# Performance work log

Hardware: AMD Instinct MI355X
Metric: run time of the kernel (lower is better)

The kernel has to match this reference:

```python
import jax, jax.numpy as jnp
import numpy as np
import math

DIM = 1024
NUM_HEADS = 16


def setup_inputs() -> dict:
    key = jax.random.key(0)
    ks = jax.random.split(key, 6)
    B, S, D = 2, 2048, DIM
    return {
        "q": jax.random.normal(ks[0], (B, S, D), dtype=jnp.float32),
        "k": jax.random.normal(ks[1], (B, S, D), dtype=jnp.float32),
        "v": jax.random.normal(ks[2], (B, S, D), dtype=jnp.float32),
        "wq": jax.random.normal(ks[3], (D, D), dtype=jnp.float32),
        "wk": jax.random.normal(ks[4], (D, D), dtype=jnp.float32),
        "wv": jax.random.normal(ks[5], (D, D), dtype=jnp.float32),
    }


def reference(q, k, v, wq, wk, wv):
    B, S, D = q.shape
    H = NUM_HEADS
    hd = D // H
    # projections: [B,S,D] @ [D,D]
    qp = (q @ wq).reshape(B, H, S, hd)  # NOTE: direct reshape, as in the original
    kp = (k @ wk).reshape(B, H, S, hd)
    vp = (v @ wv).reshape(B, H, S, hd)
    scale = 1.0 / math.sqrt(D)  # original scales by sqrt(dim), not sqrt(head_dim)
    att = jnp.einsum("bhqd,bhkd->bhqk", qp, kp) * scale  # [B,H,S,S]
    att = jax.nn.softmax(att, axis=-1)
    out = jnp.einsum("bhqk,bhkd->bhqd", att, vp)  # [B,H,S,hd]
    out = out.transpose(0, 2, 1, 3).reshape(B, S, D)
    return out
```

## Files before the change

kernel.cpp:

```cpp
#include <hip/hip_runtime.h>
#include <hip/hip_bf16.h>
#include <stdint.h>

#define DIMD 1024
#define SEQ  2048
#define NH   16
#define MROWS 4096
#define NQ   65536

typedef __bf16 bf16_t;
typedef bf16_t bf16x8 __attribute__((ext_vector_type(8)));
typedef float  f32x4  __attribute__((ext_vector_type(4)));
typedef unsigned short u16;
typedef unsigned short u16x4 __attribute__((ext_vector_type(4)));
typedef unsigned short u16x8 __attribute__((ext_vector_type(8)));
typedef unsigned int   u32;
typedef u32 u32x2 __attribute__((ext_vector_type(2)));

static __device__ __forceinline__ f32x4 mfma16(bf16x8 a, bf16x8 b, f32x4 c) {
    return __builtin_amdgcn_mfma_f32_16x16x32_bf16(a, b, c, 0, 0, 0);
}

static __device__ __forceinline__ float fast_exp2(float x) {
#if __has_builtin(__builtin_amdgcn_exp2f)
    return __builtin_amdgcn_exp2f(x);
#else
    return exp2f(x);
#endif
}

#define GLD16(gsrc, ldst) __builtin_amdgcn_global_load_lds(                    \
    (const __attribute__((address_space(1))) unsigned int*)(gsrc),             \
    (__attribute__((address_space(3))) unsigned int*)(ldst), 16, 0, 0)

static __device__ __forceinline__ void split_bf16(float x, u16& h, u16& l) {
    u32 u = __float_as_uint(x);
    u16 hu = (u16)(u >> 16);
    float xh = __uint_as_float((u32)hu << 16);
    float lo = x - xh;
    h = hu;
    l = (u16)(__float_as_uint(lo) >> 16);
}

static __device__ __forceinline__ u32 pack_bf16(float a, float b) {
    return (__float_as_uint(a) >> 16) | (__float_as_uint(b) & 0xffff0000u);
}
static __device__ __forceinline__ u32 pack_bf16_rn(float a, float b) {
    u32 ua = __float_as_uint(a) + 0x8000u;
    u32 ub = __float_as_uint(b) + 0x8000u;
    return (ua >> 16) | (ub & 0xffff0000u);
}
static __device__ __forceinline__ float bf_to_f(u16 v) {
    return __uint_as_float((u32)v << 16);
}

__global__ __launch_bounds__(256) void transWs3(
    const float* __restrict__ w0, const float* __restrict__ w1, const float* __restrict__ w2,
    u16* __restrict__ WTsH, u16* __restrict__ WTsL) {
    const int z = blockIdx.z;
    const float* W = z == 0 ? w0 : z == 1 ? w1 : w2;
    __shared__ u16 Hs[4096], Ls[4096];
    const int tid = threadIdx.x;
    const int kt = blockIdx.x, nt = blockIdx.y;
    const int n0 = nt * 128, k0 = kt * 32;
    #pragma unroll
    for (int i = 0; i < 4; i++) {
        int f = i * 256 + tid;
        int kr = f >> 5, nc4 = (f & 31) * 4;
        f32x4 w = *(const f32x4*)&W[(size_t)(k0 + kr) * DIMD + n0 + nc4];
        int cc = kr >> 3, e = kr & 7;
        #pragma unroll
        for (int j = 0; j < 4; j++) {
            u16 hh, ll; split_bf16(w[j], hh, ll);
            Hs[cc * 1024 + (nc4 + j) * 8 + e] = hh;
            Ls[cc * 1024 + (nc4 + j) * 8 + e] = ll;
        }
    }
    __syncthreads();
    const size_t base = (size_t)z * (DIMD * DIMD) + (size_t)(nt * 32 + kt) * 4096;
    #pragma unroll
    for (int i = 0; i < 2; i++) {
        int idx = (i * 256 + tid) * 8;
        *(u16x8*)(WTsH + base + idx) = *(const u16x8*)&Hs[idx];
        *(u16x8*)(WTsL + base + idx) = *(const u16x8*)&Ls[idx];
    }
}

__global__ __launch_bounds__(256, 3) void proj6(
    const float* __restrict__ xq, const float* __restrict__ xk, const float* __restrict__ xv,
    const u16* __restrict__ WTsH, const u16* __restrict__ WTsL,
    u16* __restrict__ qh, u16* __restrict__ ql,
    u16* __restrict__ kh, u16* __restrict__ kl,
    u16* __restrict__ vh) {

    const int z = blockIdx.z;
    const float* X = z == 0 ? xq : z == 1 ? xk : xv;
    const u16* BH = WTsH + (size_t)z * (DIMD * DIMD);
    const u16* BL = WTsL + (size_t)z * (DIMD * DIMD);
    u16* outH = z == 0 ? qh : z == 1 ? kh : vh;
    u16* outL = z == 0 ? ql : kl;
    const float oscale = z == 0 ? 0.0450842200278f : 1.0f;

    __shared__ u16 lds[16384];
    u16* AsH = lds;
    u16* AsL = lds + 4096;
    u16* BsH = lds + 8192;
    u16* BsL = lds + 12288;

    const int tid  = threadIdx.x;
    const int lane = tid & 63, wave = tid >> 6;
    const int quad = lane >> 4, l16 = lane & 15;
    const int wy = wave >> 1, wx = wave & 1;
    const int m0 = blockIdx.x * 128;
    const int n0 = blockIdx.y * 128;
    const size_t Bregion0 = (size_t)(blockIdx.y * 32) * 4096;

    f32x4 acc[4][4];
    #pragma unroll
    for (int mt = 0; mt < 4; mt++)
        #pragma unroll
        for (int nt = 0; nt < 4; nt++) acc[mt][nt] = (f32x4)0.0f;

    for (int kt = 0; kt < 32; kt++) {
        const int k0 = kt * 32;
        {
            const size_t rb = Bregion0 + (size_t)kt * 4096;
            int c0 = tid, c1 = 256 + tid;
            GLD16(BH + rb + c0 * 8, &BsH[c0 * 8]);
            GLD16(BH + rb + c1 * 8, &BsH[c1 * 8]);
            GLD16(BL + rb + c0 * 8, &BsL[c0 * 8]);
            GLD16(BL + rb + c1 * 8, &BsL[c1 * 8]);
        }
        #pragma unroll
        for (int i = 0; i < 4; i++) {
            int f = i * 256 + tid;
            int r = f >> 3, c4 = (f & 7) * 4;
            f32x4 a = *(const f32x4*)&X[(size_t)(m0 + r) * DIMD + k0 + c4];
            int cc = c4 >> 3, e = c4 & 7;
            u16x4 h4, l4;
            #pragma unroll
            for (int j = 0; j < 4; j++) {
                u16 hh, ll; split_bf16(a[j], hh, ll);
                h4[j] = hh; l4[j] = ll;
            }
            *(u16x4*)&AsH[(cc * 128 + r) * 8 + e] = h4;
            *(u16x4*)&AsL[(cc * 128 + r) * 8 + e] = l4;
        }
        __syncthreads();

        bf16x8 aH[4], aL[4], bH[4], bL[4];
        #pragma unroll
        for (int mt = 0; mt < 4; mt++) {
            int r = wy * 64 + mt * 16 + l16;
            aH[mt] = *(const bf16x8*)&AsH[(quad * 128 + r) * 8];
            aL[mt] = *(const bf16x8*)&AsL[(quad * 128 + r) * 8];
        }
        #pragma unroll
        for (int nt = 0; nt < 4; nt++) {
            int r = wx * 64 + nt * 16 + l16;
            bH[nt] = *(const bf16x8*)&BsH[(quad * 128 + r) * 8];
            bL[nt] = *(const bf16x8*)&BsL[(quad * 128 + r) * 8];
        }
        #pragma unroll
        for (int mt = 0; mt < 4; mt++)
            #pragma unroll
            for (int nt = 0; nt < 4; nt++) {
                acc[mt][nt] = mfma16(aH[mt], bH[nt], acc[mt][nt]);
                acc[mt][nt] = mfma16(aH[mt], bL[nt], acc[mt][nt]);
                acc[mt][nt] = mfma16(aL[mt], bH[nt], acc[mt][nt]);
            }
        __syncthreads();
    }

    #pragma unroll
    for (int mt = 0; mt < 4; mt++)
        #pragma unroll
        for (int nt = 0; nt < 4; nt++)
            #pragma unroll
            for (int r = 0; r < 4; r++) {
                int row = m0 + wy * 64 + mt * 16 + quad * 4 + r;
                int col = n0 + wx * 64 + nt * 16 + l16;
                u16 hh, ll; split_bf16(acc[mt][nt][r] * oscale, hh, ll);
                outH[(size_t)row * DIMD + col] = hh;
                if (z != 2) outL[(size_t)row * DIMD + col] = ll;
            }
}

__global__ __launch_bounds__(256) void transposeV(
    const u16* __restrict__ vh, u16* __restrict__ vt) {
    __shared__ u16 Ls[64][72];
    const int tid = threadIdx.x;
    const int bh = blockIdx.y;
    const int s0 = blockIdx.x * 64;
    const size_t slab = (size_t)bh * (SEQ * 64);
    #pragma unroll
    for (int i = 0; i < 2; i++) {
        int f = i * 256 + tid;
        int r = f >> 3, c = (f & 7) * 8;
        *(u16x8*)&Ls[r][c] = *(const u16x8*)(vh + slab + (size_t)(s0 + r) * 64 + c);
    }
    __syncthreads();
    #pragma unroll
    for (int i = 0; i < 2; i++) {
        int f = i * 256 + tid;
        int d = f >> 3, j = (f & 7) * 8;
        u16x8 o;
        #pragma unroll
        for (int jj = 0; jj < 8; jj++) o[jj] = Ls[j + jj][d];
        *(u16x8*)(vt + slab + (size_t)d * SEQ + s0 + j) = o;
    }
}

__global__ __launch_bounds__(256, 3) void flash6(
    const u16* __restrict__ qh, const u16* __restrict__ ql,
    const u16* __restrict__ kh, const u16* __restrict__ kl,
    const u16* __restrict__ vt,
    u16* __restrict__ Opart, float* __restrict__ Mpart, float* __restrict__ Lpart) {

    __shared__ u16 KH[64][72], KL[64][72], VTs[64][72];
    __shared__ u16 Ps[4][32][72];

    const int tid  = threadIdx.x;
    const int lane = tid & 63, wv = tid >> 6;
    const int quad = lane >> 4, l16 = lane & 15;
    const int bh = blockIdx.x, z = blockIdx.z;
    const size_t slab = (size_t)bh * (SEQ * 64);
    const int q0 = blockIdx.y * 128 + wv * 32;
    const int jbase = z * 1024;

    bf16x8 qfH[2][2], qfL[2][2];
    #pragma unroll
    for (int mq = 0; mq < 2; mq++) {
        const size_t rb = slab + (size_t)(q0 + mq * 16 + l16) * 64;
        #pragma unroll
        for (int kk = 0; kk < 2; kk++) {
            qfH[mq][kk] = *(const bf16x8*)(qh + rb + kk * 32 + quad * 8);
            qfL[mq][kk] = *(const bf16x8*)(ql + rb + kk * 32 + quad * 8);
        }
    }

    f32x4 O[2][4];
    float M[2] = {-3.0e38f, -3.0e38f}, L[2] = {0.0f, 0.0f};
    #pragma unroll
    for (int mq = 0; mq < 2; mq++)
        #pragma unroll
        for (int nv = 0; nv < 4; nv++) O[mq][nv] = (f32x4)0.0f;

    const int f0 = tid, f1 = 256 + tid;
    const int r0 = f0 >> 3, c0 = (f0 & 7) * 8;
    const int r1 = f1 >> 3, c1 = (f1 & 7) * 8;
    u16x8 s0, s1, s2, s3, s4, s5;

    {
        const int j0 = jbase;
        s0 = *(const u16x8*)(kh + slab + (size_t)(j0 + r0) * 64 + c0);
        s1 = *(const u16x8*)(kh + slab + (size_t)(j0 + r1) * 64 + c1);
        s2 = *(const u16x8*)(kl + slab + (size_t)(j0 + r0) * 64 + c0);
        s3 = *(const u16x8*)(kl + slab + (size_t)(j0 + r1) * 64 + c1);
        s4 = *(const u16x8*)(vt + slab + (size_t)r0 * SEQ + j0 + c0);
        s5 = *(const u16x8*)(vt + slab + (size_t)r1 * SEQ + j0 + c1);
    }
    *(u16x8*)&KH[r0][c0] = s0;  *(u16x8*)&KH[r1][c1] = s1;
    *(u16x8*)&KL[r0][c0] = s2;  *(u16x8*)&KL[r1][c1] = s3;
    *(u16x8*)&VTs[r0][c0] = s4; *(u16x8*)&VTs[r1][c1] = s5;
    __syncthreads();

    for (int t = 0; t < 16; t++) {
        if (t < 15) {
            const int j0 = jbase + (t + 1) * 64;
            s0 = *(const u16x8*)(kh + slab + (size_t)(j0 + r0) * 64 + c0);
            s1 = *(const u16x8*)(kh + slab + (size_t)(j0 + r1) * 64 + c1);
            s2 = *(const u16x8*)(kl + slab + (size_t)(j0 + r0) * 64 + c0);
            s3 = *(const u16x8*)(kl + slab + (size_t)(j0 + r1) * 64 + c1);
            s4 = *(const u16x8*)(vt + slab + (size_t)r0 * SEQ + j0 + c0);
            s5 = *(const u16x8*)(vt + slab + (size_t)r1 * SEQ + j0 + c1);
        }

        f32x4 St[2][4];
        #pragma unroll
        for (int mq = 0; mq < 2; mq++)
            #pragma unroll
            for (int nt = 0; nt < 4; nt++) St[mq][nt] = (f32x4)0.0f;
        #pragma unroll
        for (int nt = 0; nt < 4; nt++) {
            const int rB = nt * 16 + l16;
            #pragma unroll
            for (int kk = 0; kk < 2; kk++) {
                bf16x8 kHf = *(const bf16x8*)&KH[rB][kk * 32 + quad * 8];
                bf16x8 kLf = *(const bf16x8*)&KL[rB][kk * 32 + quad * 8];
                #pragma unroll
                for (int mq = 0; mq < 2; mq++) {
                    St[mq][nt] = mfma16(kHf, qfH[mq][kk], St[mq][nt]);
                    St[mq][nt] = mfma16(kLf, qfH[mq][kk], St[mq][nt]);
                    St[mq][nt] = mfma16(kHf, qfL[mq][kk], St[mq][nt]);
                }
            }
        }

        #pragma unroll
        for (int mq = 0; mq < 2; mq++) {
            float mx = St[mq][0][0];
            #pragma unroll
            for (int nt = 0; nt < 4; nt++)
                #pragma unroll
                for (int r = 0; r < 4; r++) mx = fmaxf(mx, St[mq][nt][r]);
            mx = fmaxf(mx, __shfl_xor(mx, 16));
            mx = fmaxf(mx, __shfl_xor(mx, 32));
            float Mn = M[mq];
            if (__any(mx > Mn)) {
                Mn = fmaxf(Mn, mx);
                float al = fast_exp2(M[mq] - Mn);
                M[mq] = Mn;
                L[mq] *= al;
                #pragma unroll
                for (int nv = 0; nv < 4; nv++) O[mq][nv] *= al;
            }
            float rs = 0.0f;
            #pragma unroll
            for (int nt = 0; nt < 4; nt++)
                #pragma unroll
                for (int r = 0; r < 4; r++) {
                    float p = fast_exp2(St[mq][nt][r] - Mn);
                    St[mq][nt][r] = p;
                    rs += p;
                }
            rs += __shfl_xor(rs, 16);
            rs += __shfl_xor(rs, 32);
            L[mq] += rs;
            #pragma unroll
            for (int nt = 0; nt < 4; nt++) {
                u32x2 d;
                d[0] = pack_bf16(St[mq][nt][0], St[mq][nt][1]);
                d[1] = pack_bf16(St[mq][nt][2], St[mq][nt][3]);
                *(u32x2*)&Ps[wv][mq * 16 + l16][nt * 16 + quad * 4] = d;
            }
        }

        #pragma unroll
        for (int kk = 0; kk < 2; kk++) {
            bf16x8 pB[2];
            #pragma unroll
            for (int mq = 0; mq < 2; mq++)
                pB[mq] = *(const bf16x8*)&Ps[wv][mq * 16 + l16][kk * 32 + quad * 8];
            #pragma unroll
            for (int nv = 0; nv < 4; nv++) {
                bf16x8 vF = *(const bf16x8*)&VTs[nv * 16 + l16][kk * 32 + quad * 8];
                #pragma unroll
                for (int mq = 0; mq < 2; mq++)
                    O[mq][nv] = mfma16(vF, pB[mq], O[mq][nv]);
            }
        }

        __syncthreads();
        if (t < 15) {
            *(u16x8*)&KH[r0][c0] = s0;  *(u16x8*)&KH[r1][c1] = s1;
            *(u16x8*)&KL[r0][c0] = s2;  *(u16x8*)&KL[r1][c1] = s3;
            *(u16x8*)&VTs[r0][c0] = s4; *(u16x8*)&VTs[r1][c1] = s5;
        }
        __syncthreads();
    }

    const int qgb = bh * SEQ + q0;
    #pragma unroll
    for (int mq = 0; mq < 2; mq++) {
        const int qg = qgb + mq * 16 + l16;
        #pragma unroll
        for (int nv = 0; nv < 4; nv++) {
            u32x2 d;
            d[0] = pack_bf16_rn(O[mq][nv][0], O[mq][nv][1]);
            d[1] = pack_bf16_rn(O[mq][nv][2], O[mq][nv][3]);
            *(u32x2*)(Opart + ((size_t)(z * NQ + qg)) * 64 + nv * 16 + quad * 4) = d;
        }
        if (quad == 0) {
            Mpart[z * NQ + qg] = M[mq];
            Lpart[z * NQ + qg] = L[mq];
        }
    }
}

__global__ __launch_bounds__(256) void combineK(
    const u16* __restrict__ Opart, const float* __restrict__ Mpart,
    const float* __restrict__ Lpart, float* __restrict__ out) {
    int idx = blockIdx.x * 256 + threadIdx.x;
    int qg = idx >> 4, c4 = (idx & 15) * 4;
    float M0 = Mpart[qg], M1 = Mpart[NQ + qg];
    float L0 = Lpart[qg], L1 = Lpart[NQ + qg];
    float Ms = fmaxf(M0, M1);
    float w0 = fast_exp2(M0 - Ms), w1 = fast_exp2(M1 - Ms);
    float inv = 1.0f / (w0 * L0 + w1 * L1);
    u16x4 a = *(const u16x4*)&Opart[(size_t)qg * 64 + c4];
    u16x4 b = *(const u16x4*)&Opart[((size_t)NQ + qg) * 64 + c4];
    f32x4 o;
    #pragma unroll
    for (int j = 0; j < 4; j++)
        o[j] = (w0 * bf_to_f(a[j]) + w1 * bf_to_f(b[j])) * inv;
    int bh = qg >> 11, s = qg & 2047;
    int bb = bh >> 4, h = bh & 15;
    *(f32x4*)&out[((size_t)(bb * SEQ + s)) * DIMD + h * 64 + c4] = o;
}

extern "C" void kernel_launch(void* const* d_in, const int* in_sizes, int n_in,
                              void* d_out, int out_size, void* d_ws, size_t ws_size,
                              hipStream_t stream) {
    const float* q  = (const float*)d_in[0];
    const float* k  = (const float*)d_in[1];
    const float* v  = (const float*)d_in[2];
    const float* wq = (const float*)d_in[3];
    const float* wk = (const float*)d_in[4];
    const float* wv = (const float*)d_in[5];
    float* out = (float*)d_out;

    char* ws = (char*)d_ws;
    const size_t MB = 1 << 20;
    u16* qh   = (u16*)(ws + 0 * MB);
    u16* ql   = (u16*)(ws + 8 * MB);
    u16* kh   = (u16*)(ws + 16 * MB);
    u16* kl   = (u16*)(ws + 24 * MB);
    u16* vh   = (u16*)(ws + 32 * MB);
    u16* vt   = (u16*)(ws + 40 * MB);
    u16* WTsH = (u16*)(ws + 48 * MB);
    u16* WTsL = (u16*)(ws + 54 * MB);
    u16*   Opart = (u16*)(ws + 48 * MB);
    float* Mpart = (float*)(ws + 64 * MB);
    float* Lpart = (float*)(ws + 64 * MB + 512 * 1024);

    transWs3<<<dim3(32, 8, 3), 256, 0, stream>>>(wq, wk, wv, WTsH, WTsL);

    proj6<<<dim3(32, 8, 3), 256, 0, stream>>>(
        q, k, v, WTsH, WTsL, qh, ql, kh, kl, vh);

    transposeV<<<dim3(SEQ / 64, 2 * NH), 256, 0, stream>>>(vh, vt);

    flash6<<<dim3(2 * NH, SEQ / 128, 2), 256, 0, stream>>>(
        qh, ql, kh, kl, vt, Opart, Mpart, Lpart);

    combineK<<<dim3(NQ * 16 / 256), 256, 0, stream>>>(Opart, Mpart, Lpart, out);
}
```

Baseline: 270.5 us.

## Double-buffer projection GEMM loads, swizzle A tile LDS, prioritise flash MFMA waves

The projection kernel now prefetches the next K-slice of X into registers and stages the next weight tile into a second LDS buffer while the current tile's MFMAs run. The A tile gets an XOR-swizzled LDS layout to reduce bank conflicts. The flash attention kernel raises wave priority around its MFMA blocks. This adds LDS use (48KB per block), which may lower occupancy under the 3-block launch bound, plus extra register pressure from the prefetched A values.

```diff
diff --git a/kernel.cpp b/kernel.cpp
--- a/kernel.cpp
+++ b/kernel.cpp
@@ -86,7 +86,7 @@
     }
 }
 
-__global__ __launch_bounds__(256, 3) void proj6(
+__global__ __launch_bounds__(256, 3) void proj7(
     const float* __restrict__ xq, const float* __restrict__ xk, const float* __restrict__ xv,
     const u16* __restrict__ WTsH, const u16* __restrict__ WTsL,
     u16* __restrict__ qh, u16* __restrict__ ql,
@@ -101,11 +101,9 @@
     u16* outL = z == 0 ? ql : kl;
     const float oscale = z == 0 ? 0.0450842200278f : 1.0f;
 
-    __shared__ u16 lds[16384];
+    __shared__ u16 lds[24576];
     u16* AsH = lds;
     u16* AsL = lds + 4096;
-    u16* BsH = lds + 8192;
-    u16* BsL = lds + 12288;
 
     const int tid  = threadIdx.x;
     const int lane = tid & 63, wave = tid >> 6;
@@ -115,45 +113,80 @@
     const int n0 = blockIdx.y * 128;
     const size_t Bregion0 = (size_t)(blockIdx.y * 32) * 4096;
 
+    const int rA  = tid >> 2, ccA = tid & 3;
+    const int idxA0 = ccA * 1024 + ((rA ^ (ccA << 1)) * 8);
+    const int idxA1 = idxA0 + 512;
+    const float* Xb0 = X + (size_t)(m0 + rA) * DIMD + ccA * 8;
+    const float* Xb1 = X + (size_t)(m0 + rA + 64) * DIMD + ccA * 8;
+
     f32x4 acc[4][4];
     #pragma unroll
     for (int mt = 0; mt < 4; mt++)
         #pragma unroll
         for (int nt = 0; nt < 4; nt++) acc[mt][nt] = (f32x4)0.0f;
 
+    f32x4 pa0, pa1, pa2, pa3;
+
+#define LOADA(kt) do {                                                         \
+        pa0 = *(const f32x4*)(Xb0 + (kt) * 32);                                \
+        pa1 = *(const f32x4*)(Xb0 + (kt) * 32 + 4);                            \
+        pa2 = *(const f32x4*)(Xb1 + (kt) * 32);                                \
+        pa3 = *(const f32x4*)(Xb1 + (kt) * 32 + 4);                            \
+    } while (0)
+
+#define WRITEA() do {                                                          \
+        u16x8 h, l;                                                            \
+        _Pragma("unroll")                                                      \
+        for (int j = 0; j < 4; j++) {                                          \
+            u16 hh, ll;                                                        \
+            split_bf16(pa0[j], hh, ll); h[j] = hh;     l[j] = ll;              \
+            split_bf16(pa1[j], hh, ll); h[4 + j] = hh; l[4 + j] = ll;          \
+        }                                                                      \
+        *(u16x8*)&AsH[idxA0] = h;                                              \
+        *(u16x8*)&AsL[idxA0] = l;                                              \
+        _Pragma("unroll")                                                      \
+        for (int j = 0; j < 4; j++) {                                          \
+            u16 hh, ll;                                                        \
+            split_bf16(pa2[j], hh, ll); h[j] = hh;     l[j] = ll;              \
+            split_bf16(pa3[j], hh, ll); h[4 + j] = hh; l[4 + j] = ll;          \
+        }                                                                      \
+        *(u16x8*)&AsH[idxA1] = h;                                              \
+        *(u16x8*)&AsL[idxA1] = l;                                              \
+    } while (0)
+
+#define STAGEB(kt, buf) do {                                                   \
+        const size_t rb = Bregion0 + (size_t)(kt) * 4096;                      \
+        u16* BsHd = lds + 8192 + (buf) * 8192;                                 \
+        u16* BsLd = BsHd + 4096;                                               \
+        int c0 = tid, c1 = 256 + tid;                                          \
+        GLD16(BH + rb + c0 * 8, &BsHd[c0 * 8]);                                \
+        GLD16(BH + rb + c1 * 8, &BsHd[c1 * 8]);                                \
+        GLD16(BL + rb + c0 * 8, &BsLd[c0 * 8]);                                \
+        GLD16(BL + rb + c1 * 8, &BsLd[c1 * 8]);                                \
+    } while (0)
+
+    LOADA(0);
+    STAGEB(0, 0);
+    WRITEA();
+    __syncthreads();
+
     for (int kt = 0; kt < 32; kt++) {
-        const int k0 = kt * 32;
-        {
-            const size_t rb = Bregion0 + (size_t)kt * 4096;
-            int c0 = tid, c1 = 256 + tid;
-            GLD16(BH + rb + c0 * 8, &BsH[c0 * 8]);
-            GLD16(BH + rb + c1 * 8, &BsH[c1 * 8]);
-            GLD16(BL + rb + c0 * 8, &BsL[c0 * 8]);
-            GLD16(BL + rb + c1 * 8, &BsL[c1 * 8]);
-        }
-        #pragma unroll
-        for (int i = 0; i < 4; i++) {
-            int f = i * 256 + tid;
-            int r = f >> 3, c4 = (f & 7) * 4;
-            f32x4 a = *(const f32x4*)&X[(size_t)(m0 + r) * DIMD + k0 + c4];
-            int cc = c4 >> 3, e = c4 & 7;
-            u16x4 h4, l4;
-            #pragma unroll
-            for (int j = 0; j < 4; j++) {
-                u16 hh, ll; split_bf16(a[j], hh, ll);
-                h4[j] = hh; l4[j] = ll;
-            }
-            *(u16x4*)&AsH[(cc * 128 + r) * 8 + e] = h4;
-            *(u16x4*)&AsL[(cc * 128 + r) * 8 + e] = l4;
-        }
-        __syncthreads();
+        const int cur = kt & 1;
+        if (kt < 31) {
+            LOADA(kt + 1);
+            STAGEB(kt + 1, cur ^ 1);
+        }
+
+        const u16* BsH = lds + 8192 + cur * 8192;
+        const u16* BsL = BsH + 4096;
 
         bf16x8 aH[4], aL[4], bH[4], bL[4];
         #pragma unroll
         for (int mt = 0; mt < 4; mt++) {
             int r = wy * 64 + mt * 16 + l16;
-            aH[mt] = *(const bf16x8*)&AsH[(quad * 128 + r) * 8];
-            aL[mt] = *(const bf16x8*)&AsL[(quad * 128 + r) * 8];
+            int idx = quad * 1024 + ((r ^ (quad << 1)) * 8);
+            aH[mt] = *(const bf16x8*)&AsH[idx];
+            aL[mt] = *(const bf16x8*)&AsL[idx];
         }
         #pragma unroll
         for (int nt = 0; nt < 4; nt++) {
@@ -169,8 +202,14 @@
                 acc[mt][nt] = mfma16(aH[mt], bL[nt], acc[mt][nt]);
                 acc[mt][nt] = mfma16(aL[mt], bH[nt], acc[mt][nt]);
             }
+
         __syncthreads();
-    }
+        if (kt < 31) WRITEA();
+        __syncthreads();
+    }
+#undef LOADA
+#undef WRITEA
+#undef STAGEB
 
     #pragma unroll
     for (int mt = 0; mt < 4; mt++)
@@ -281,6 +320,7 @@
         for (int mq = 0; mq < 2; mq++)
             #pragma unroll
             for (int nt = 0; nt < 4; nt++) St[mq][nt] = (f32x4)0.0f;
+        __builtin_amdgcn_s_setprio(1);
         #pragma unroll
         for (int nt = 0; nt < 4; nt++) {
             const int rB = nt * 16 + l16;
@@ -296,6 +336,7 @@
                 }
             }
         }
+        __builtin_amdgcn_s_setprio(0);
 
         #pragma unroll
         for (int mq = 0; mq < 2; mq++) {
@@ -336,6 +377,7 @@
             }
         }
 
+        __builtin_amdgcn_s_setprio(1);
         #pragma unroll
         for (int kk = 0; kk < 2; kk++) {
             bf16x8 pB[2];
@@ -350,6 +392,7 @@
                     O[mq][nv] = mfma16(vF, pB[mq], O[mq][nv]);
             }
         }
+        __builtin_amdgcn_s_setprio(0);
 
         __syncthreads();
         if (t < 15) {
@@ -426,7 +469,7 @@
 
     transWs3<<<dim3(32, 8, 3), 256, 0, stream>>>(wq, wk, wv, WTsH, WTsL);
 
-    proj6<<<dim3(32, 8, 3), 256, 0, stream>>>(
+    proj7<<<dim3(32, 8, 3), 256, 0, stream>>>(
         q, k, v, WTsH, WTsL, qh, ql, kh, kl, vh);
 
     transposeV<<<dim3(SEQ / 64, 2 * NH), 256, 0, stream>>>(vh, vt);
```

After: 265.8 us. About the same (-1.8%).
